# Kernel optimization log

Hardware: AMD Instinct MI355X
Metric: run time of the kernel (lower is better)

Reference implementation:

```python
import jax, jax.numpy as jnp
import numpy as np

B, T, D = 8, 4096, 256
GATE_MIN, GATE_MAX = 0.01, 0.99


def setup_inputs() -> dict:
    key = jax.random.key(0)
    ks = jax.random.split(key, 8)
    inp = {
        "x_re": jax.random.normal(ks[0], (B, T, D), jnp.float32),
        "x_im": jax.random.normal(ks[1], (B, T, D), jnp.float32),
        "s0_re": jnp.zeros((B, D), jnp.float32),
        "s0_im": jnp.zeros((B, D), jnp.float32),
        "decay_re": jax.random.normal(ks[2], (D,), jnp.float32),
        "decay_im": 0.1 * jax.random.normal(ks[3], (D,), jnp.float32),
        "Wm": 0.02 * jax.random.normal(ks[4], (2 * D, 2 * D), jnp.float32)
              + jnp.eye(2 * D, dtype=jnp.float32),  # eye_ init on diag blocks
        "bm": jnp.zeros((2 * D,), jnp.float32),
        "Wo": 0.02 * jax.random.normal(ks[5], (2 * D, 2 * D), jnp.float32),
        "bo": jnp.zeros((2 * D,), jnp.float32),
        "Wg": 0.02 * jax.random.normal(ks[6], (D, 2 * D), jnp.float32),
        "bg": jnp.zeros((D,), jnp.float32),
    }
    return inp


def reference(x_re, x_im, s0_re, s0_im, decay_re, decay_im,
              Wm, bm, Wo, bo, Wg, bg):
    # decay = sigmoid(decay_re) + i*decay_im
    dr = jax.nn.sigmoid(decay_re)
    di = decay_im

    # scan over time: inputs as [T, B, D]
    xs = (jnp.swapaxes(x_re, 0, 1), jnp.swapaxes(x_im, 0, 1))

    def step(carry, xt):
        s_re, s_im = carry
        xr, xi = xt                                   # [B, D]
        x_cat = jnp.concatenate([xr, xi], axis=-1)    # [B, 2D]
        x_in = x_cat @ Wm.T + bm
        ur, ui = jnp.split(x_in, 2, axis=-1)
        # complex mul-add: new_state = prev_state * decay + update
        ns_re = s_re * dr - s_im * di + ur
        ns_im = s_re * di + s_im * dr + ui
        s_cat = jnp.concatenate([ns_re, ns_im], axis=-1)  # [B, 2D]
        source = s_cat @ Wo.T + bo                        # [B, 2D] (re|im)
        gate = jnp.clip(jax.nn.sigmoid(s_cat @ Wg.T + bg), GATE_MIN, GATE_MAX)
        y = jnp.concatenate([source, gate], axis=-1)      # [B, 3D]
        return (ns_re, ns_im), y

    _, ys = jax.lax.scan(step, (s0_re, s0_im), xs)        # [T, B, 3D]
    return jnp.swapaxes(ys, 0, 1)                          # [B, T, 3D] = [src_re|src_im|gate]
```

## Files before the change

### kernel.cpp

```cpp
#include <hip/hip_runtime.h>
#include <hip/hip_bf16.h>
#include <cstdint>
#include <cstddef>


typedef __bf16 bf16;
typedef __bf16 bf16x8 __attribute__((ext_vector_type(8)));
typedef float floatx4 __attribute__((ext_vector_type(4)));

#define NB 8
#define NT 4096
#define ND 256
#define BT (NB * NT)
#define TWOD 512
#define CHUNK 32
#define NCHUNK (NT / CHUNK)

static __device__ __forceinline__ float sigmoidf_(float x) {
  return 1.0f / (1.0f + __expf(-x));
}

static __device__ __forceinline__ void async_copy16(const void* g, void* l) {
  __builtin_amdgcn_global_load_lds(
      (__attribute__((address_space(1))) void*)g,
      (__attribute__((address_space(3))) void*)l, 16, 0, 0);
}

union U32BF2 { unsigned int u; __bf16 h[2]; };

__global__ void k_prep(const float* __restrict__ Wm,
                       const float* __restrict__ bm,
                       const float* __restrict__ Wo,
                       const float* __restrict__ Wg,
                       const float* __restrict__ bo,
                       const float* __restrict__ bg,
                       bf16* __restrict__ Wm_b,
                       bf16* __restrict__ Wc_b,
                       float* __restrict__ bm_p,
                       float* __restrict__ bc) {
  const int i = blockIdx.x * 256 + threadIdx.x;
  {
    const int r = i >> 9, c = i & 511;
    const int sr = (r >> 1) + (r & 1) * 256;
    Wm_b[i] = (bf16)Wm[sr * 512 + c];
  }
  {
    const int r = i >> 9, c = i & 511;
    const int sc = (c >> 1) + (c & 1) * 256;
    Wc_b[i] = (bf16)Wo[r * 512 + sc];
    if (i < 131072) Wc_b[262144 + i] = (bf16)Wg[r * 512 + sc];
  }
  if (i < 512) { bm_p[i] = bm[(i >> 1) + (i & 1) * 256]; bc[i] = bo[i]; }
  if (i < 256) bc[512 + i] = bg[i];
}

__global__ __launch_bounds__(256) void gemm1(
    const float* __restrict__ xre, const float* __restrict__ xim,
    const bf16* __restrict__ Bw, const float* __restrict__ bias,
    bf16* __restrict__ C) {
  __shared__ __align__(16) bf16 As[128 * 64];
  __shared__ __align__(16) bf16 Bs[128 * 64];
  const int tid = threadIdx.x;
  const int wave = tid >> 6;
  const int lane = tid & 63;
  const int quad = lane >> 4;
  const int l16 = lane & 15;
  const int m0 = blockIdx.x * 128;
  const int n0 = blockIdx.y * 128;
  const int wm = (wave >> 1) * 64;
  const int wn = (wave & 1) * 64;
  const int srow = lane >> 3;
  const int schunk = (lane & 7) ^ (srow & 7);
  const int ar = tid >> 3;
  const int sg = tid & 7;

  floatx4 acc[4][4];
#pragma unroll
  for (int i = 0; i < 4; ++i)
#pragma unroll
    for (int j = 0; j < 4; ++j) acc[i][j] = (floatx4)0.0f;

  for (int k0 = 0; k0 < 512; k0 += 64) {
    const float* xs = (k0 < 256) ? xre : xim;
    const int xcol = k0 & 255;
    __syncthreads();
#pragma unroll
    for (int i = 0; i < 4; ++i) {
      const int seg = wave * 4 + i;
      const int row = seg * 8 + srow;
      async_copy16(Bw + (size_t)(n0 + row) * 512 + k0 + schunk * 8, Bs + seg * 512);
    }
#pragma unroll
    for (int it = 0; it < 4; ++it) {
      const int r = ar + 32 * it;
      const int cg = sg ^ (r & 7);
      const float* src = xs + (size_t)(m0 + r) * 256 + xcol + cg * 8;
      const float4 f0 = *(const float4*)(src);
      const float4 f1 = *(const float4*)(src + 4);
      bf16x8 v;
      v[0] = (bf16)f0.x; v[1] = (bf16)f0.y; v[2] = (bf16)f0.z; v[3] = (bf16)f0.w;
      v[4] = (bf16)f1.x; v[5] = (bf16)f1.y; v[6] = (bf16)f1.z; v[7] = (bf16)f1.w;
      *(bf16x8*)(As + r * 64 + sg * 8) = v;
    }
    __syncthreads();

#pragma unroll
    for (int s = 0; s < 2; ++s) {
      bf16x8 af[4], bfr[4];
#pragma unroll
      for (int mi = 0; mi < 4; ++mi) {
        const int row = wm + mi * 16 + l16;
        const int ch = ((s << 2) | quad) ^ (l16 & 7);
        af[mi] = *(const bf16x8*)(As + row * 64 + ch * 8);
      }
#pragma unroll
      for (int ni = 0; ni < 4; ++ni) {
        const int row = wn + ni * 16 + l16;
        const int ch = ((s << 2) | quad) ^ (l16 & 7);
        bfr[ni] = *(const bf16x8*)(Bs + row * 64 + ch * 8);
      }
#pragma unroll
      for (int mi = 0; mi < 4; ++mi)
#pragma unroll
        for (int ni = 0; ni < 4; ++ni)
          acc[mi][ni] = __builtin_amdgcn_mfma_f32_16x16x32_bf16(
              af[mi], bfr[ni], acc[mi][ni], 0, 0, 0);
    }
  }

#pragma unroll
  for (int mi = 0; mi < 4; ++mi) {
    const int rb = m0 + wm + mi * 16 + quad * 4;
#pragma unroll
    for (int ni = 0; ni < 4; ++ni) {
      const int col = n0 + wn + ni * 16 + l16;
      const float bb = bias[col];
#pragma unroll
      for (int r = 0; r < 4; ++r)
        C[(size_t)(rb + r) * TWOD + col] = (bf16)(acc[mi][ni][r] + bb);
    }
  }
}

__global__ __launch_bounds__(256) void gemm2(
    const bf16* __restrict__ A, const bf16* __restrict__ Bw,
    const float* __restrict__ bias, float* __restrict__ C) {
  __shared__ __align__(16) bf16 As[128 * 64];
  __shared__ __align__(16) bf16 Bs[64 * 64];
  const int tid = threadIdx.x;
  const int wave = tid >> 6;
  const int lane = tid & 63;
  const int quad = lane >> 4;
  const int l16 = lane & 15;
  const int m0 = blockIdx.x * 128;
  const int n0 = blockIdx.y * 64;
  const int wm = (wave >> 1) * 64;
  const int wn = (wave & 1) * 32;
  const int srow = lane >> 3;
  const int schunk = (lane & 7) ^ (srow & 7);

  floatx4 acc[4][2];
#pragma unroll
  for (int i = 0; i < 4; ++i)
#pragma unroll
    for (int j = 0; j < 2; ++j) acc[i][j] = (floatx4)0.0f;

  for (int k0 = 0; k0 < 512; k0 += 64) {
    __syncthreads();
#pragma unroll
    for (int i = 0; i < 4; ++i) {
      const int seg = wave * 4 + i;
      const int row = seg * 8 + srow;
      async_copy16(A + (size_t)(m0 + row) * 512 + k0 + schunk * 8, As + seg * 512);
    }
#pragma unroll
    for (int i = 0; i < 2; ++i) {
      const int seg = wave * 2 + i;
      const int row = seg * 8 + srow;
      async_copy16(Bw + (size_t)(n0 + row) * 512 + k0 + schunk * 8, Bs + seg * 512);
    }
    __syncthreads();

#pragma unroll
    for (int s = 0; s < 2; ++s) {
      bf16x8 af[4], bfr[2];
#pragma unroll
      for (int mi = 0; mi < 4; ++mi) {
        const int row = wm + mi * 16 + l16;
        const int ch = ((s << 2) | quad) ^ (l16 & 7);
        af[mi] = *(const bf16x8*)(As + row * 64 + ch * 8);
      }
#pragma unroll
      for (int ni = 0; ni < 2; ++ni) {
        const int row = wn + ni * 16 + l16;
        const int ch = ((s << 2) | quad) ^ (l16 & 7);
        bfr[ni] = *(const bf16x8*)(Bs + row * 64 + ch * 8);
      }
#pragma unroll
      for (int mi = 0; mi < 4; ++mi)
#pragma unroll
        for (int ni = 0; ni < 2; ++ni)
          acc[mi][ni] = __builtin_amdgcn_mfma_f32_16x16x32_bf16(
              af[mi], bfr[ni], acc[mi][ni], 0, 0, 0);
    }
  }

#pragma unroll
  for (int mi = 0; mi < 4; ++mi) {
    const int rb = m0 + wm + mi * 16 + quad * 4;
#pragma unroll
    for (int ni = 0; ni < 2; ++ni) {
      const int col = n0 + wn + ni * 16 + l16;
      const float bb = bias[col];
#pragma unroll
      for (int r = 0; r < 4; ++r) {
        float v = acc[mi][ni][r] + bb;
        if (col >= 512) v = fminf(fmaxf(sigmoidf_(v), 0.01f), 0.99f);
        C[(size_t)(rb + r) * 768 + col] = v;
      }
    }
  }
}

__global__ void k_scan_pass1(const bf16* __restrict__ U,
                             const float* __restrict__ decay_re,
                             const float* __restrict__ decay_im,
                             float* __restrict__ Fre, float* __restrict__ Fim) {
  const int d = threadIdx.x;
  const int c = blockIdx.x;
  const int b = blockIdx.y;
  const float dr = sigmoidf_(decay_re[d]);
  const float di = decay_im[d];
  float sr = 0.f, si = 0.f;
  const unsigned int* Ur = (const unsigned int*)
      (U + ((size_t)b * NT + (size_t)c * CHUNK) * TWOD + 2 * d);
#pragma unroll 4
  for (int j = 0; j < CHUNK; ++j) {
    U32BF2 cv; cv.u = Ur[(size_t)j * (TWOD / 2)];
    const float ur = (float)cv.h[0];
    const float ui = (float)cv.h[1];
    const float nr = sr * dr - si * di + ur;
    const float ni = sr * di + si * dr + ui;
    sr = nr; si = ni;
  }
  const int o = (b * NCHUNK + c) * ND + d;
  Fre[o] = sr; Fim[o] = si;
}

__global__ void k_scan_pass2(const float* __restrict__ Fre,
                             const float* __restrict__ Fim,
                             const float* __restrict__ s0_re,
                             const float* __restrict__ s0_im,
                             const float* __restrict__ decay_re,
                             const float* __restrict__ decay_im,
                             float* __restrict__ Ire, float* __restrict__ Iim) {
  const int d = threadIdx.x;
  const int b = blockIdx.x;
  const float dr = sigmoidf_(decay_re[d]);
  const float di = decay_im[d];
  float pr = dr, pi = di;
#pragma unroll
  for (int i = 0; i < 5; ++i) {
    const float nr = pr * pr - pi * pi;
    const float ni = 2.f * pr * pi;
    pr = nr; pi = ni;
  }
  float sr = s0_re[b * ND + d];
  float si = s0_im[b * ND + d];
  for (int c = 0; c < NCHUNK; ++c) {
    const int o = (b * NCHUNK + c) * ND + d;
    Ire[o] = sr; Iim[o] = si;
    const float nr = sr * pr - si * pi + Fre[o];
    const float ni = sr * pi + si * pr + Fim[o];
    sr = nr; si = ni;
  }
}

__global__ void k_scan_pass3(bf16* __restrict__ U,
                             const float* __restrict__ decay_re,
                             const float* __restrict__ decay_im,
                             const float* __restrict__ Ire,
                             const float* __restrict__ Iim) {
  const int d = threadIdx.x;
  const int c = blockIdx.x;
  const int b = blockIdx.y;
  const float dr = sigmoidf_(decay_re[d]);
  const float di = decay_im[d];
  const int o = (b * NCHUNK + c) * ND + d;
  float sr = Ire[o], si = Iim[o];
  unsigned int* Ur = (unsigned int*)
      (U + ((size_t)b * NT + (size_t)c * CHUNK) * TWOD + 2 * d);
#pragma unroll 4
  for (int j = 0; j < CHUNK; ++j) {
    U32BF2 cv; cv.u = Ur[(size_t)j * (TWOD / 2)];
    const float ur = (float)cv.h[0];
    const float ui = (float)cv.h[1];
    const float nr = sr * dr - si * di + ur;
    const float ni = sr * di + si * dr + ui;
    sr = nr; si = ni;
    cv.h[0] = (bf16)nr; cv.h[1] = (bf16)ni;
    Ur[(size_t)j * (TWOD / 2)] = cv.u;
  }
}


extern "C" void kernel_launch(void* const* d_in, const int* in_sizes, int n_in,
                              void* d_out, int out_size, void* d_ws, size_t ws_size,
                              hipStream_t stream) {
  const float* x_re = (const float*)d_in[0];
  const float* x_im = (const float*)d_in[1];
  const float* s0_re = (const float*)d_in[2];
  const float* s0_im = (const float*)d_in[3];
  const float* decay_re = (const float*)d_in[4];
  const float* decay_im = (const float*)d_in[5];
  const float* Wm = (const float*)d_in[6];
  const float* bm = (const float*)d_in[7];
  const float* Wo = (const float*)d_in[8];
  const float* bo = (const float*)d_in[9];
  const float* Wg = (const float*)d_in[10];
  const float* bg = (const float*)d_in[11];

  char* ws = (char*)d_ws;
  const size_t U_OFF = 0;
  const size_t WM_OFF = 33554432;
  const size_t WC_OFF = WM_OFF + 524288;
  const size_t BMP_OFF = WC_OFF + 786432;
  const size_t BC_OFF = BMP_OFF + 4096;
  const size_t FRE_OFF = BC_OFF + 4096;
  const size_t FIM_OFF = FRE_OFF + 1048576;
  const size_t IRE_OFF = FIM_OFF + 1048576;
  const size_t IIM_OFF = IRE_OFF + 1048576;

  bf16* U = (bf16*)(ws + U_OFF);
  bf16* Wm_b = (bf16*)(ws + WM_OFF);
  bf16* Wc_b = (bf16*)(ws + WC_OFF);
  float* bm_p = (float*)(ws + BMP_OFF);
  float* bc = (float*)(ws + BC_OFF);
  float* Fre = (float*)(ws + FRE_OFF);
  float* Fim = (float*)(ws + FIM_OFF);
  float* Ire = (float*)(ws + IRE_OFF);
  float* Iim = (float*)(ws + IIM_OFF);

  k_prep<<<dim3(1024), 256, 0, stream>>>(Wm, bm, Wo, Wg, bo, bg,
                                         Wm_b, Wc_b, bm_p, bc);
  gemm1<<<dim3(256, 4), 256, 0, stream>>>(x_re, x_im, Wm_b, bm_p, U);
  k_scan_pass1<<<dim3(NCHUNK, NB), ND, 0, stream>>>(U, decay_re, decay_im, Fre, Fim);
  k_scan_pass2<<<dim3(NB), ND, 0, stream>>>(Fre, Fim, s0_re, s0_im,
                                            decay_re, decay_im, Ire, Iim);
  k_scan_pass3<<<dim3(NCHUNK, NB), ND, 0, stream>>>(U, decay_re, decay_im, Ire, Iim);
  gemm2<<<dim3(256, 12), 256, 0, stream>>>(U, Wc_b, bc, (float*)d_out);
}
```

Measured before the change: 259.8 us.

## Fuse chunk-local scan into gemm1 epilogue and parallelize cross-chunk scan

gemm1 now stages its output tile in shared memory, writes it out with coalesced 16-byte stores, and computes the per-chunk local scan totals (pass1) from that tile, so the separate pass1 kernel and its re-read of U are gone. The serial per-batch cross-chunk scan (pass2, 8 blocks looping 128 chunks) becomes a parallel Hillis-Steele scan with one block per (d, batch) and one thread per chunk. This removes a kernel launch and a full read of U and shortens the serial dependency chain. In exchange gemm1 uses more shared memory and does extra epilogue work, and the parallel scan can change rounding order.

```diff
diff --git a/kernel.cpp b/kernel.cpp
--- a/kernel.cpp
+++ b/kernel.cpp
@@ -57,9 +57,13 @@
 __global__ __launch_bounds__(256) void gemm1(
     const float* __restrict__ xre, const float* __restrict__ xim,
     const bf16* __restrict__ Bw, const float* __restrict__ bias,
-    bf16* __restrict__ C) {
-  __shared__ __align__(16) bf16 As[128 * 64];
-  __shared__ __align__(16) bf16 Bs[128 * 64];
+    bf16* __restrict__ Cu,
+    const float* __restrict__ decay_re, const float* __restrict__ decay_im,
+    float* __restrict__ Fre, float* __restrict__ Fim) {
+  __shared__ __align__(16) bf16 smem[128 * 128];
+  bf16* As = smem;
+  bf16* Bs = smem + 128 * 64;
+  bf16* Us = smem;
   const int tid = threadIdx.x;
   const int wave = tid >> 6;
   const int lane = tid & 63;
@@ -128,152 +132,104 @@
     }
   }
 
+  __syncthreads();
 #pragma unroll
   for (int mi = 0; mi < 4; ++mi) {
-    const int rb = m0 + wm + mi * 16 + quad * 4;
+    const int rloc = wm + mi * 16 + quad * 4;
 #pragma unroll
     for (int ni = 0; ni < 4; ++ni) {
-      const int col = n0 + wn + ni * 16 + l16;
-      const float bb = bias[col];
+      const int cloc = wn + ni * 16 + l16;
+      const float bb = bias[n0 + cloc];
 #pragma unroll
       for (int r = 0; r < 4; ++r)
-        C[(size_t)(rb + r) * TWOD + col] = (bf16)(acc[mi][ni][r] + bb);
-    }
-  }
-}
-
-__global__ __launch_bounds__(256) void gemm2(
-    const bf16* __restrict__ A, const bf16* __restrict__ Bw,
-    const float* __restrict__ bias, float* __restrict__ C) {
-  __shared__ __align__(16) bf16 As[128 * 64];
-  __shared__ __align__(16) bf16 Bs[64 * 64];
-  const int tid = threadIdx.x;
-  const int wave = tid >> 6;
-  const int lane = tid & 63;
-  const int quad = lane >> 4;
-  const int l16 = lane & 15;
-  const int m0 = blockIdx.x * 128;
-  const int n0 = blockIdx.y * 64;
-  const int wm = (wave >> 1) * 64;
-  const int wn = (wave & 1) * 32;
-  const int srow = lane >> 3;
-  const int schunk = (lane & 7) ^ (srow & 7);
-
-  floatx4 acc[4][2];
-#pragma unroll
-  for (int i = 0; i < 4; ++i)
-#pragma unroll
-    for (int j = 0; j < 2; ++j) acc[i][j] = (floatx4)0.0f;
-
-  for (int k0 = 0; k0 < 512; k0 += 64) {
-    __syncthreads();
-#pragma unroll
-    for (int i = 0; i < 4; ++i) {
-      const int seg = wave * 4 + i;
-      const int row = seg * 8 + srow;
-      async_copy16(A + (size_t)(m0 + row) * 512 + k0 + schunk * 8, As + seg * 512);
-    }
-#pragma unroll
-    for (int i = 0; i < 2; ++i) {
-      const int seg = wave * 2 + i;
-      const int row = seg * 8 + srow;
-      async_copy16(Bw + (size_t)(n0 + row) * 512 + k0 + schunk * 8, Bs + seg * 512);
-    }
-    __syncthreads();
-
-#pragma unroll
-    for (int s = 0; s < 2; ++s) {
-      bf16x8 af[4], bfr[2];
-#pragma unroll
-      for (int mi = 0; mi < 4; ++mi) {
-        const int row = wm + mi * 16 + l16;
-        const int ch = ((s << 2) | quad) ^ (l16 & 7);
-        af[mi] = *(const bf16x8*)(As + row * 64 + ch * 8);
-      }
-#pragma unroll
-      for (int ni = 0; ni < 2; ++ni) {
-        const int row = wn + ni * 16 + l16;
-        const int ch = ((s << 2) | quad) ^ (l16 & 7);
-        bfr[ni] = *(const bf16x8*)(Bs + row * 64 + ch * 8);
-      }
-#pragma unroll
-      for (int mi = 0; mi < 4; ++mi)
-#pragma unroll
-        for (int ni = 0; ni < 2; ++ni)
-          acc[mi][ni] = __builtin_amdgcn_mfma_f32_16x16x32_bf16(
-              af[mi], bfr[ni], acc[mi][ni], 0, 0, 0);
-    }
-  }
-
-#pragma unroll
-  for (int mi = 0; mi < 4; ++mi) {
-    const int rb = m0 + wm + mi * 16 + quad * 4;
-#pragma unroll
-    for (int ni = 0; ni < 2; ++ni) {
-      const int col = n0 + wn + ni * 16 + l16;
-      const float bb = bias[col];
-#pragma unroll
-      for (int r = 0; r < 4; ++r) {
-        float v = acc[mi][ni][r] + bb;
-        if (col >= 512) v = fminf(fmaxf(sigmoidf_(v), 0.01f), 0.99f);
-        C[(size_t)(rb + r) * 768 + col] = v;
-      }
-    }
-  }
-}
-
-__global__ void k_scan_pass1(const bf16* __restrict__ U,
-                             const float* __restrict__ decay_re,
-                             const float* __restrict__ decay_im,
-                             float* __restrict__ Fre, float* __restrict__ Fim) {
-  const int d = threadIdx.x;
-  const int c = blockIdx.x;
+        Us[(rloc + r) * 128 + cloc] = (bf16)(acc[mi][ni][r] + bb);
+    }
+  }
+  __syncthreads();
+  {
+    bf16* dst = Cu + (size_t)m0 * TWOD + n0;
+#pragma unroll
+    for (int i = 0; i < 8; ++i) {
+      const int e = i * 256 + tid;
+      const int row = e >> 4, ch = e & 15;
+      *(bf16x8*)(dst + (size_t)row * TWOD + ch * 8) =
+          *(const bf16x8*)(Us + row * 128 + ch * 8);
+    }
+  }
+  {
+    const int sc = tid >> 6;
+    const int dd = tid & 63;
+    const int d = (n0 >> 1) + dd;
+    const float drr = sigmoidf_(decay_re[d]);
+    const float dii = decay_im[d];
+    float sr = 0.f, si = 0.f;
+    const unsigned int* Up = (const unsigned int*)(Us + (sc * 32) * 128 + 2 * dd);
+#pragma unroll 4
+    for (int j = 0; j < 32; ++j) {
+      U32BF2 cv; cv.u = Up[j * 64];
+      const float ur = (float)cv.h[0];
+      const float ui = (float)cv.h[1];
+      const float nr = sr * drr - si * dii + ur;
+      const float ni2 = sr * dii + si * drr + ui;
+      sr = nr; si = ni2;
+    }
+    const int bidx = m0 >> 12;
+    const int cchunk = ((m0 & 4095) >> 5) + sc;
+    const int o = (bidx * NCHUNK + cchunk) * ND + d;
+    Fre[o] = sr; Fim[o] = si;
+  }
+}
+
+__global__ void k_scan2(const float* __restrict__ Fre,
+                        const float* __restrict__ Fim,
+                        const float* __restrict__ s0_re,
+                        const float* __restrict__ s0_im,
+                        const float* __restrict__ decay_re,
+                        const float* __restrict__ decay_im,
+                        float* __restrict__ Ire, float* __restrict__ Iim) {
+  const int c = threadIdx.x;
+  const int d = blockIdx.x;
   const int b = blockIdx.y;
-  const float dr = sigmoidf_(decay_re[d]);
-  const float di = decay_im[d];
-  float sr = 0.f, si = 0.f;
-  const unsigned int* Ur = (const unsigned int*)
-      (U + ((size_t)b * NT + (size_t)c * CHUNK) * TWOD + 2 * d);
-#pragma unroll 4
-  for (int j = 0; j < CHUNK; ++j) {
-    U32BF2 cv; cv.u = Ur[(size_t)j * (TWOD / 2)];
-    const float ur = (float)cv.h[0];
-    const float ui = (float)cv.h[1];
-    const float nr = sr * dr - si * di + ur;
-    const float ni = sr * di + si * dr + ui;
-    sr = nr; si = ni;
+  const float drr = sigmoidf_(decay_re[d]);
+  const float dii = decay_im[d];
+  float wr = drr, wi = dii;
+#pragma unroll
+  for (int i = 0; i < 5; ++i) {
+    const float nr = wr * wr - wi * wi;
+    const float ni = 2.f * wr * wi;
+    wr = nr; wi = ni;
   }
   const int o = (b * NCHUNK + c) * ND + d;
-  Fre[o] = sr; Fim[o] = si;
-}
-
-__global__ void k_scan_pass2(const float* __restrict__ Fre,
-                             const float* __restrict__ Fim,
-                             const float* __restrict__ s0_re,
-                             const float* __restrict__ s0_im,
-                             const float* __restrict__ decay_re,
-                             const float* __restrict__ decay_im,
-                             float* __restrict__ Ire, float* __restrict__ Iim) {
-  const int d = threadIdx.x;
-  const int b = blockIdx.x;
-  const float dr = sigmoidf_(decay_re[d]);
-  const float di = decay_im[d];
-  float pr = dr, pi = di;
-#pragma unroll
-  for (int i = 0; i < 5; ++i) {
-    const float nr = pr * pr - pi * pi;
-    const float ni = 2.f * pr * pi;
-    pr = nr; pi = ni;
-  }
-  float sr = s0_re[b * ND + d];
-  float si = s0_im[b * ND + d];
-  for (int c = 0; c < NCHUNK; ++c) {
-    const int o = (b * NCHUNK + c) * ND + d;
-    Ire[o] = sr; Iim[o] = si;
-    const float nr = sr * pr - si * pi + Fre[o];
-    const float ni = sr * pi + si * pr + Fim[o];
-    sr = nr; si = ni;
-  }
+  float vr = Fre[o], vi = Fim[o];
+  float ar = 1.f, ai = 0.f;
+  __shared__ float lr[128], li[128];
+#pragma unroll
+  for (int k = 1; k < 128; k <<= 1) {
+    lr[c] = vr; li[c] = vi;
+    __syncthreads();
+    const float tr = (c >= k) ? lr[c - k] : 0.f;
+    const float ti = (c >= k) ? li[c - k] : 0.f;
+    __syncthreads();
+    vr += wr * tr - wi * ti;
+    vi += wr * ti + wi * tr;
+    if (c & k) {
+      const float nar = ar * wr - ai * wi;
+      ai = ar * wi + ai * wr;
+      ar = nar;
+    }
+    const float nwr = wr * wr - wi * wi;
+    wi = 2.f * wr * wi;
+    wr = nwr;
+  }
+  lr[c] = vr; li[c] = vi;
+  __syncthreads();
+  float er = (c > 0) ? lr[c - 1] : 0.f;
+  float ei = (c > 0) ? li[c - 1] : 0.f;
+  const float s0r = s0_re[b * ND + d];
+  const float s0i = s0_im[b * ND + d];
+  er += ar * s0r - ai * s0i;
+  ei += ar * s0i + ai * s0r;
+  Ire[o] = er; Iim[o] = ei;
 }
 
 __global__ void k_scan_pass3(bf16* __restrict__ U,
@@ -303,6 +259,86 @@
   }
 }
 
+__global__ __launch_bounds__(256) void gemm2(
+    const bf16* __restrict__ A, const bf16* __restrict__ Bw,
+    const float* __restrict__ bias, float* __restrict__ C) {
+  __shared__ __align__(16) bf16 As[128 * 64];
+  __shared__ __align__(16) bf16 Bs[64 * 64];
+  const int tid = threadIdx.x;
+  const int wave = tid >> 6;
+  const int lane = tid & 63;
+  const int quad = lane >> 4;
+  const int l16 = lane & 15;
+  const int m0 = blockIdx.x * 128;
+  const int n0 = blockIdx.y * 64;
+  const int wm = (wave >> 1) * 64;
+  const int wn = (wave & 1) * 32;
+  const int srow = lane >> 3;
+  const int schunk = (lane & 7) ^ (srow & 7);
+
+  floatx4 acc[4][2];
+#pragma unroll
+  for (int i = 0; i < 4; ++i)
+#pragma unroll
+    for (int j = 0; j < 2; ++j) acc[i][j] = (floatx4)0.0f;
+
+  for (int k0 = 0; k0 < 512; k0 += 64) {
+    __syncthreads();
+#pragma unroll
+    for (int i = 0; i < 4; ++i) {
+      const int seg = wave * 4 + i;
+      const int row = seg * 8 + srow;
+      async_copy16(A + (size_t)(m0 + row) * 512 + k0 + schunk * 8, As + seg * 512);
+    }
+#pragma unroll
+    for (int i = 0; i < 2; ++i) {
+      const int seg = wave * 2 + i;
+      const int row = seg * 8 + srow;
+      async_copy16(Bw + (size_t)(n0 + row) * 512 + k0 + schunk * 8, Bs + seg * 512);
+    }
+    __syncthreads();
+
+#pragma unroll
+    for (int s = 0; s < 2; ++s) {
+      bf16x8 af[4], bfr[2];
+#pragma unroll
+      for (int mi = 0; mi < 4; ++mi) {
+        const int row = wm + mi * 16 + l16;
+        const int ch = ((s << 2) | quad) ^ (l16 & 7);
+        af[mi] = *(const bf16x8*)(As + row * 64 + ch * 8);
+      }
+#pragma unroll
+      for (int ni = 0; ni < 2; ++ni) {
+        const int row = wn + ni * 16 + l16;
+        const int ch = ((s << 2) | quad) ^ (l16 & 7);
+        bfr[ni] = *(const bf16x8*)(Bs + row * 64 + ch * 8);
+      }
+#pragma unroll
+      for (int mi = 0; mi < 4; ++mi)
+#pragma unroll
+        for (int ni = 0; ni < 2; ++ni)
+          acc[mi][ni] = __builtin_amdgcn_mfma_f32_16x16x32_bf16(
+              af[mi], bfr[ni], acc[mi][ni], 0, 0, 0);
+    }
+  }
+
+#pragma unroll
+  for (int mi = 0; mi < 4; ++mi) {
+    const int rb = m0 + wm + mi * 16 + quad * 4;
+#pragma unroll
+    for (int ni = 0; ni < 2; ++ni) {
+      const int col = n0 + wn + ni * 16 + l16;
+      const float bb = bias[col];
+#pragma unroll
+      for (int r = 0; r < 4; ++r) {
+        float v = acc[mi][ni][r] + bb;
+        if (col >= 512) v = fminf(fmaxf(sigmoidf_(v), 0.01f), 0.99f);
+        C[(size_t)(rb + r) * 768 + col] = v;
+      }
+    }
+  }
+}
+
 
 extern "C" void kernel_launch(void* const* d_in, const int* in_sizes, int n_in,
                               void* d_out, int out_size, void* d_ws, size_t ws_size,
@@ -343,10 +379,10 @@
 
   k_prep<<<dim3(1024), 256, 0, stream>>>(Wm, bm, Wo, Wg, bo, bg,
                                          Wm_b, Wc_b, bm_p, bc);
-  gemm1<<<dim3(256, 4), 256, 0, stream>>>(x_re, x_im, Wm_b, bm_p, U);
-  k_scan_pass1<<<dim3(NCHUNK, NB), ND, 0, stream>>>(U, decay_re, decay_im, Fre, Fim);
-  k_scan_pass2<<<dim3(NB), ND, 0, stream>>>(Fre, Fim, s0_re, s0_im,
-                                            decay_re, decay_im, Ire, Iim);
+  gemm1<<<dim3(256, 4), 256, 0, stream>>>(x_re, x_im, Wm_b, bm_p, U,
+                                          decay_re, decay_im, Fre, Fim);
+  k_scan2<<<dim3(ND, NB), NCHUNK, 0, stream>>>(Fre, Fim, s0_re, s0_im,
+                                               decay_re, decay_im, Ire, Iim);
   k_scan_pass3<<<dim3(NCHUNK, NB), ND, 0, stream>>>(U, decay_re, decay_im, Ire, Iim);
   gemm2<<<dim3(256, 12), 256, 0, stream>>>(U, Wc_b, bc, (float*)d_out);
 }
```

New measurement: 254.0 us. 1.02x faster.
